# Optimization experiments

Measured on AMD Instinct MI355X. Metric: run time of the kernel, lower is better.

## Reference

```python
import jax, jax.numpy as jnp
import numpy as np

IMG = 2048
STRIDES = [8, 16, 32, 64, 128]
A = 9                       # num_cell_anchors
CLASS_NUM = 16              # num_classes - 1
TOPK = 1000                 # config.test_layer_topk
MAX_DELTA = float(np.log(1000.0 / 16.0))

_LEVEL_N = [(IMG // s) * (IMG // s) * A for s in STRIDES]


def setup_inputs() -> dict:
    key = jax.random.key(0)
    inp = {}
    for l, n in enumerate(_LEVEL_N):
        key, k1, k2, k3, k4 = jax.random.split(key, 5)
        cxcy = jax.random.uniform(k1, (n, 2), minval=0.0, maxval=float(IMG))
        wh = jax.random.uniform(k2, (n, 2), minval=8.0, maxval=128.0)
        inp[f"anchors{l}"] = jnp.concatenate([cxcy - 0.5 * wh, cxcy + 0.5 * wh], axis=1)
        # logits biased negative like a trained RetinaNet cls head (prior_prob init)
        inp[f"cls{l}"] = jax.random.normal(k3, (1, n, CLASS_NUM), dtype=jnp.float32) - 4.0
        inp[f"reg{l}"] = jax.random.normal(k4, (1, n, 8), dtype=jnp.float32) * 0.1
    return inp


def bbox_transform_inv(rois, deltas):
    # standard box decode (restore_bbox with unnormalize=False)
    w = rois[:, 2] - rois[:, 0]
    h = rois[:, 3] - rois[:, 1]
    cx = rois[:, 0] + 0.5 * w
    cy = rois[:, 1] + 0.5 * h
    pcx = cx + deltas[:, 0] * w
    pcy = cy + deltas[:, 1] * h
    pw = w * jnp.exp(jnp.minimum(deltas[:, 2], MAX_DELTA))
    ph = h * jnp.exp(jnp.minimum(deltas[:, 3], MAX_DELTA))
    return jnp.stack([pcx - 0.5 * pw, pcy - 0.5 * ph,
                      pcx + 0.5 * pw, pcy + 0.5 * ph], axis=1)


def _per_layer(anchors, pred_cls, pred_reg):
    a = anchors.reshape(-1, 4)
    c = pred_cls[0].reshape(-1, CLASS_NUM)
    r = pred_reg[0].reshape(-1, 8)[:, :4]
    if a.shape[0] > TOPK:
        ruler = jnp.max(c, axis=1)                  # max score over classes
        _, inds = jax.lax.top_k(ruler, TOPK)        # irregular topk + gather
        a = jnp.take(a, inds, axis=0)
        c = jnp.take(c, inds, axis=0)
        r = jnp.take(r, inds, axis=0)
    return a, jax.nn.sigmoid(c), r


def reference(anchors0, cls0, reg0, anchors1, cls1, reg1, anchors2, cls2, reg2,
              anchors3, cls3, reg3, anchors4, cls4, reg4):
    levels = [(anchors0, cls0, reg0), (anchors1, cls1, reg1),
              (anchors2, cls2, reg2), (anchors3, cls3, reg3),
              (anchors4, cls4, reg4)]
    kept = [_per_layer(a, c, r) for a, c, r in levels]
    keep_anchors = jnp.concatenate([k[0] for k in kept], axis=0)   # [K,4]
    keep_cls = jnp.concatenate([k[1] for k in kept], axis=0)       # [K,C]
    keep_reg = jnp.concatenate([k[2] for k in kept], axis=0)       # [K,4]
    K = keep_cls.shape[0]
    tag = jnp.tile(jnp.arange(CLASS_NUM, dtype=keep_cls.dtype) + 1.0, (K,)).reshape(-1, 1)
    pred_scores = keep_cls.reshape(-1, 1)                          # [K*C,1]
    pred_bbox = bbox_transform_inv(keep_anchors, keep_reg)         # [K,4]
    pred_bbox = jnp.tile(pred_bbox, (1, CLASS_NUM)).reshape(-1, 4) # [K*C,4]
    return jnp.concatenate([pred_bbox, pred_scores, tag], axis=1)  # [K*C,6]
```

## Files before the change

### kernel.cpp

```cpp
#include <hip/hip_runtime.h>
#include <math.h>

#define NLEV 5
#define TOPKK 1000
#define NCLS 16
#define NPART 16
#define PART_CAP 256
#define CAND_TOT 2048
#define NTOT 785664u
#define HISTSZ (NLEV * 256)

__device__ __forceinline__ int find_level(unsigned i, unsigned& loc) {
    if (i < 589824u) { loc = i;            return 0; }
    if (i < 737280u) { loc = i - 589824u;  return 1; }
    if (i < 774144u) { loc = i - 737280u;  return 2; }
    if (i < 783360u) { loc = i - 774144u;  return 3; }
    loc = i - 783360u; return 4;
}

struct Ptrs {
    const float* anc[NLEV];
    const float* cls[NLEV];
    const float* reg[NLEV];
};

__device__ __forceinline__ unsigned f2key(float f) {
    unsigned u = __float_as_uint(f);
    return (u & 0x80000000u) ? ~u : (u | 0x80000000u);
}

__device__ __forceinline__ float max4(float4 v) {
    return fmaxf(fmaxf(v.x, v.y), fmaxf(v.z, v.w));
}

__global__ void k_keys_hist(Ptrs p, unsigned* keys, unsigned* hist) {
    __shared__ unsigned lh[HISTSZ];
    for (int t = threadIdx.x; t < HISTSZ; t += blockDim.x) lh[t] = 0u;
    __syncthreads();
    unsigned i = blockIdx.x * blockDim.x + threadIdx.x;
    if (i < NTOT) {
        unsigned loc; int l = find_level(i, loc);
        const float4* c = (const float4*)(p.cls[l]) + (size_t)loc * 4;
        float4 a = c[0], b = c[1], d = c[2], e = c[3];
        float m = max4(a);
        m = fmaxf(m, max4(b));
        m = fmaxf(m, max4(d));
        m = fmaxf(m, max4(e));
        unsigned k = f2key(m);
        keys[i] = k;
        atomicAdd(&lh[l * 256 + (k >> 24)], 1u);
    }
    __syncthreads();
    unsigned part = blockIdx.x & (NPART - 1);
    for (int t = threadIdx.x; t < HISTSZ; t += blockDim.x)
        if (lh[t]) atomicAdd(&hist[part * HISTSZ + t], lh[t]);
}

__global__ void k_hist2(const unsigned* keys, const unsigned* prefix, unsigned* hist) {
    __shared__ unsigned lh[HISTSZ];
    __shared__ unsigned pf[NLEV];
    for (int t = threadIdx.x; t < HISTSZ; t += blockDim.x) lh[t] = 0u;
    if (threadIdx.x < NLEV) pf[threadIdx.x] = prefix[threadIdx.x];
    __syncthreads();
    unsigned i = blockIdx.x * blockDim.x + threadIdx.x;
    if (i < NTOT) {
        unsigned loc; int l = find_level(i, loc);
        unsigned k = keys[i];
        if ((k & 0xFF000000u) == pf[l])
            atomicAdd(&lh[l * 256 + ((k >> 16) & 0xFFu)], 1u);
    }
    __syncthreads();
    unsigned part = blockIdx.x & (NPART - 1);
    for (int t = threadIdx.x; t < HISTSZ; t += blockDim.x)
        if (lh[t]) atomicAdd(&hist[part * HISTSZ + t], lh[t]);
}

__global__ void k_select(unsigned* hist, unsigned* prefix, unsigned* remaining,
                         int shift, int first, unsigned* zbuf, unsigned zn) {
    __shared__ unsigned s[256];
    int l = blockIdx.x;
    int t = threadIdx.x, r = 255 - t;
    unsigned c = 0;
    #pragma unroll
    for (int pp = 0; pp < NPART; pp++) c += hist[pp * HISTSZ + l * 256 + t];
    s[r] = c;
    __syncthreads();
    for (int d = 1; d < 256; d <<= 1) {
        unsigned v = (r >= d) ? s[r - d] : 0u;
        __syncthreads();
        s[r] += v;
        __syncthreads();
    }
    unsigned incl = s[r], above = incl - c;
    unsigned rem = first ? (unsigned)TOPKK : remaining[l];
    unsigned pf = first ? 0u : prefix[l];
    if (above < rem && rem <= incl) {
        prefix[l] = pf | (((unsigned)t) << shift);
        remaining[l] = rem - above;
    }
    for (unsigned i = blockIdx.x * 256u + t; i < zn; i += NLEV * 256u)
        zbuf[i] = 0u;
}

__global__ void k_compact(const unsigned* keys, const unsigned* prefix,
                          unsigned* cnt, unsigned long long* cand) {
    unsigned i = blockIdx.x * blockDim.x + threadIdx.x;
    if (i >= NTOT) return;
    unsigned loc; int l = find_level(i, loc);
    unsigned k = keys[i];
    if (k >= prefix[l]) {
        unsigned part = blockIdx.x & (NPART - 1);
        unsigned slot = atomicAdd(&cnt[l * NPART + part], 1u);
        if (slot < PART_CAP)
            cand[((size_t)(l * NPART + part)) * PART_CAP + slot] =
                ((unsigned long long)k << 32) | (unsigned)(~loc);
    }
}

__global__ __launch_bounds__(256) void k_rank_emit(Ptrs p, const unsigned* cnt,
                                                   const unsigned long long* cand,
                                                   float* out) {
    const float MAXD = 4.135166556742356f;
    int l = blockIdx.x >> 3;
    unsigned sl = blockIdx.x & 7;
    int t = threadIdx.x;
    __shared__ unsigned long long lbuf[CAND_TOT];
    __shared__ unsigned aux[33];

    if (t < NPART) {
        unsigned cc = cnt[l * NPART + t];
        aux[t] = (cc > PART_CAP) ? PART_CAP : cc;
    }
    __syncthreads();
    if (t == 0) {
        unsigned o = 0;
        for (int pp = 0; pp < NPART; pp++) { aux[16 + pp] = o; o += aux[pp]; }
        aux[32] = (o > CAND_TOT) ? CAND_TOT : o;
    }
    __syncthreads();
    unsigned n = aux[32];
    for (int pp = 0; pp < NPART; pp++) {
        unsigned cc = aux[pp], o = aux[16 + pp];
        for (unsigned e = t; e < cc; e += 256) {
            unsigned dst = o + e;
            if (dst < CAND_TOT)
                lbuf[dst] = cand[((size_t)(l * NPART + pp)) * PART_CAP + e];
        }
    }
    __syncthreads();

    unsigned j = sl * 256u + t;
    if (j >= n) return;
    unsigned long long my = lbuf[j];
    unsigned rank = 0;
    #pragma unroll 8
    for (unsigned q = 0; q < n; q++) rank += (lbuf[q] > my) ? 1u : 0u;
    if (rank >= TOPKK) return;

    unsigned idx = ~((unsigned)(my & 0xFFFFFFFFull));
    float4 an = ((const float4*)p.anc[l])[idx];
    float4 dd = ((const float4*)p.reg[l])[(size_t)idx * 2];
    float w = an.z - an.x, h = an.w - an.y;
    float cx = an.x + 0.5f * w, cy = an.y + 0.5f * h;
    float pcx = cx + dd.x * w, pcy = cy + dd.y * h;
    float pw = w * expf(fminf(dd.z, MAXD));
    float ph = h * expf(fminf(dd.w, MAXD));
    float bx = pcx - 0.5f * pw, by = pcy - 0.5f * ph;
    float bz = pcx + 0.5f * pw, bw = pcy + 0.5f * ph;

    const float4* cp = (const float4*)(p.cls[l]) + (size_t)idx * 4;
    float sg[16];
    #pragma unroll
    for (int g = 0; g < 4; g++) {
        float4 v = cp[g];
        sg[4 * g + 0] = 1.0f / (1.0f + expf(-v.x));
        sg[4 * g + 1] = 1.0f / (1.0f + expf(-v.y));
        sg[4 * g + 2] = 1.0f / (1.0f + expf(-v.z));
        sg[4 * g + 3] = 1.0f / (1.0f + expf(-v.w));
    }
    float4* q = (float4*)(out + (size_t)(l * TOPKK + rank) * (NCLS * 6));
    #pragma unroll
    for (int g = 0; g < 8; g++) {
        float ta = (float)(2 * g + 1), tb = (float)(2 * g + 2);
        q[3 * g + 0] = make_float4(bx, by, bz, bw);
        q[3 * g + 1] = make_float4(sg[2 * g], ta, bx, by);
        q[3 * g + 2] = make_float4(bz, bw, sg[2 * g + 1], tb);
    }
}

extern "C" void kernel_launch(void* const* d_in, const int* in_sizes, int n_in,
                              void* d_out, int out_size, void* d_ws, size_t ws_size,
                              hipStream_t stream) {
    Ptrs p;
    for (int l = 0; l < NLEV; l++) {
        p.anc[l] = (const float*)d_in[3 * l + 0];
        p.cls[l] = (const float*)d_in[3 * l + 1];
        p.reg[l] = (const float*)d_in[3 * l + 2];
    }
    char* w = (char*)d_ws;
    unsigned* keys      = (unsigned*)w;
    unsigned* histA     = (unsigned*)(w + 3142656);
    unsigned* histB     = (unsigned*)(w + 3224576);
    unsigned long long* cand = (unsigned long long*)(w + 3306496);
    unsigned* prefix    = (unsigned*)(w + 3470336);
    unsigned* remaining = (unsigned*)(w + 3470368);
    unsigned* cnt       = (unsigned*)(w + 3470400);

    float* out = (float*)d_out;
    int nb = (NTOT + 255) / 256;

    (void)hipMemsetAsync(histA, 0, 81920, stream);
    k_keys_hist<<<nb, 256, 0, stream>>>(p, keys, histA);
    k_select<<<NLEV, 256, 0, stream>>>(histA, prefix, remaining, 24, 1,
                                       histB, HISTSZ * NPART);
    k_hist2<<<nb, 256, 0, stream>>>(keys, prefix, histB);
    k_select<<<NLEV, 256, 0, stream>>>(histB, prefix, remaining, 16, 0,
                                       cnt, NLEV * NPART);
    k_compact<<<nb, 256, 0, stream>>>(keys, prefix, cnt, cand);
    k_rank_emit<<<NLEV * 8, 256, 0, stream>>>(p, cnt, cand, out);
}
```

Baseline: 195.9 us.

## Fold radix-select scans into histogram and compaction kernels, dropping two select launches

Removes the two small single-wave k_select launches. Each block of the hist2 and compact kernels now redundantly recomputes the per-level prefix scan from the global histograms. One memset clears histA, histB and the counters together. Because every level size is a multiple of 256, each block belongs to exactly one level, so the local histogram shrinks to 256 bins and the bounds checks go away. The cost is that every one of about three thousand blocks reads 16x256 histogram entries and runs a 256-wide scan, twice in compact.

```diff
diff --git a/kernel.cpp b/kernel.cpp
--- a/kernel.cpp
+++ b/kernel.cpp
@@ -33,56 +33,13 @@
     return fmaxf(fmaxf(v.x, v.y), fmaxf(v.z, v.w));
 }
 
-__global__ void k_keys_hist(Ptrs p, unsigned* keys, unsigned* hist) {
-    __shared__ unsigned lh[HISTSZ];
-    for (int t = threadIdx.x; t < HISTSZ; t += blockDim.x) lh[t] = 0u;
-    __syncthreads();
-    unsigned i = blockIdx.x * blockDim.x + threadIdx.x;
-    if (i < NTOT) {
-        unsigned loc; int l = find_level(i, loc);
-        const float4* c = (const float4*)(p.cls[l]) + (size_t)loc * 4;
-        float4 a = c[0], b = c[1], d = c[2], e = c[3];
-        float m = max4(a);
-        m = fmaxf(m, max4(b));
-        m = fmaxf(m, max4(d));
-        m = fmaxf(m, max4(e));
-        unsigned k = f2key(m);
-        keys[i] = k;
-        atomicAdd(&lh[l * 256 + (k >> 24)], 1u);
-    }
-    __syncthreads();
-    unsigned part = blockIdx.x & (NPART - 1);
-    for (int t = threadIdx.x; t < HISTSZ; t += blockDim.x)
-        if (lh[t]) atomicAdd(&hist[part * HISTSZ + t], lh[t]);
-}
-
-__global__ void k_hist2(const unsigned* keys, const unsigned* prefix, unsigned* hist) {
-    __shared__ unsigned lh[HISTSZ];
-    __shared__ unsigned pf[NLEV];
-    for (int t = threadIdx.x; t < HISTSZ; t += blockDim.x) lh[t] = 0u;
-    if (threadIdx.x < NLEV) pf[threadIdx.x] = prefix[threadIdx.x];
-    __syncthreads();
-    unsigned i = blockIdx.x * blockDim.x + threadIdx.x;
-    if (i < NTOT) {
-        unsigned loc; int l = find_level(i, loc);
-        unsigned k = keys[i];
-        if ((k & 0xFF000000u) == pf[l])
-            atomicAdd(&lh[l * 256 + ((k >> 16) & 0xFFu)], 1u);
-    }
-    __syncthreads();
-    unsigned part = blockIdx.x & (NPART - 1);
-    for (int t = threadIdx.x; t < HISTSZ; t += blockDim.x)
-        if (lh[t]) atomicAdd(&hist[part * HISTSZ + t], lh[t]);
-}
-
-__global__ void k_select(unsigned* hist, unsigned* prefix, unsigned* remaining,
-                         int shift, int first, unsigned* zbuf, unsigned zn) {
-    __shared__ unsigned s[256];
-    int l = blockIdx.x;
+__device__ void level_select(const unsigned* histbase, int l, int shift,
+                             unsigned rem_in, unsigned pf_acc,
+                             unsigned* s, unsigned* aux) {
     int t = threadIdx.x, r = 255 - t;
     unsigned c = 0;
     #pragma unroll
-    for (int pp = 0; pp < NPART; pp++) c += hist[pp * HISTSZ + l * 256 + t];
+    for (int pp = 0; pp < NPART; pp++) c += histbase[pp * HISTSZ + l * 256 + t];
     s[r] = c;
     __syncthreads();
     for (int d = 1; d < 256; d <<= 1) {
@@ -92,23 +49,73 @@
         __syncthreads();
     }
     unsigned incl = s[r], above = incl - c;
-    unsigned rem = first ? (unsigned)TOPKK : remaining[l];
-    unsigned pf = first ? 0u : prefix[l];
-    if (above < rem && rem <= incl) {
-        prefix[l] = pf | (((unsigned)t) << shift);
-        remaining[l] = rem - above;
-    }
-    for (unsigned i = blockIdx.x * 256u + t; i < zn; i += NLEV * 256u)
-        zbuf[i] = 0u;
-}
-
-__global__ void k_compact(const unsigned* keys, const unsigned* prefix,
-                          unsigned* cnt, unsigned long long* cand) {
-    unsigned i = blockIdx.x * blockDim.x + threadIdx.x;
-    if (i >= NTOT) return;
+    if (above < rem_in && rem_in <= incl) {
+        aux[0] = pf_acc | (((unsigned)t) << shift);
+        aux[1] = rem_in - above;
+    }
+    __syncthreads();
+}
+
+__global__ __launch_bounds__(256) void k_keys_hist(Ptrs p, unsigned* keys,
+                                                   unsigned* hist) {
+    __shared__ unsigned lh[256];
+    lh[threadIdx.x] = 0u;
+    __syncthreads();
+    unsigned i = blockIdx.x * 256u + threadIdx.x;
     unsigned loc; int l = find_level(i, loc);
-    unsigned k = keys[i];
-    if (k >= prefix[l]) {
+    const float4* c = (const float4*)(p.cls[l]) + (size_t)loc * 4;
+    float4 a = c[0], b = c[1], d = c[2], e = c[3];
+    float m = max4(a);
+    m = fmaxf(m, max4(b));
+    m = fmaxf(m, max4(d));
+    m = fmaxf(m, max4(e));
+    unsigned k = f2key(m);
+    keys[i] = k;
+    atomicAdd(&lh[k >> 24], 1u);
+    __syncthreads();
+    unsigned part = blockIdx.x & (NPART - 1);
+    if (lh[threadIdx.x])
+        atomicAdd(&hist[part * HISTSZ + l * 256 + threadIdx.x], lh[threadIdx.x]);
+}
+
+__global__ __launch_bounds__(256) void k_hist2(const unsigned* keys,
+                                               const unsigned* histA,
+                                               unsigned* histB) {
+    __shared__ unsigned s[256];
+    __shared__ unsigned lh[256];
+    __shared__ unsigned aux[2];
+    unsigned i0 = blockIdx.x * 256u;
+    unsigned loc0; int l = find_level(i0, loc0);
+    level_select(histA, l, 24, TOPKK, 0u, s, aux);
+    unsigned pf = aux[0];
+    lh[threadIdx.x] = 0u;
+    __syncthreads();
+    unsigned k = keys[i0 + threadIdx.x];
+    if ((k & 0xFF000000u) == pf)
+        atomicAdd(&lh[(k >> 16) & 0xFFu], 1u);
+    __syncthreads();
+    unsigned part = blockIdx.x & (NPART - 1);
+    if (lh[threadIdx.x])
+        atomicAdd(&histB[part * HISTSZ + l * 256 + threadIdx.x], lh[threadIdx.x]);
+}
+
+__global__ __launch_bounds__(256) void k_compact(const unsigned* keys,
+                                                 const unsigned* histA,
+                                                 const unsigned* histB,
+                                                 unsigned* cnt,
+                                                 unsigned long long* cand) {
+    __shared__ unsigned s[256];
+    __shared__ unsigned aux[2];
+    unsigned i0 = blockIdx.x * 256u;
+    unsigned loc0; int l = find_level(i0, loc0);
+    level_select(histA, l, 24, TOPKK, 0u, s, aux);
+    unsigned pf1 = aux[0], rem1 = aux[1];
+    __syncthreads();
+    level_select(histB, l, 16, rem1, pf1, s, aux);
+    unsigned thresh = aux[0];
+    unsigned k = keys[i0 + threadIdx.x];
+    if (k >= thresh) {
+        unsigned loc = loc0 + threadIdx.x;
         unsigned part = blockIdx.x & (NPART - 1);
         unsigned slot = atomicAdd(&cnt[l * NPART + part], 1u);
         if (slot < PART_CAP)
@@ -198,24 +205,18 @@
         p.reg[l] = (const float*)d_in[3 * l + 2];
     }
     char* w = (char*)d_ws;
-    unsigned* keys      = (unsigned*)w;
-    unsigned* histA     = (unsigned*)(w + 3142656);
-    unsigned* histB     = (unsigned*)(w + 3224576);
-    unsigned long long* cand = (unsigned long long*)(w + 3306496);
-    unsigned* prefix    = (unsigned*)(w + 3470336);
-    unsigned* remaining = (unsigned*)(w + 3470368);
-    unsigned* cnt       = (unsigned*)(w + 3470400);
+    unsigned* keys  = (unsigned*)w;
+    unsigned* histA = (unsigned*)(w + 3142656);
+    unsigned* histB = (unsigned*)(w + 3224576);
+    unsigned* cnt   = (unsigned*)(w + 3306496);
+    unsigned long long* cand = (unsigned long long*)(w + 3306816);
 
     float* out = (float*)d_out;
-    int nb = (NTOT + 255) / 256;
-
-    (void)hipMemsetAsync(histA, 0, 81920, stream);
+    int nb = NTOT / 256;
+
+    (void)hipMemsetAsync(histA, 0, 164160, stream);
     k_keys_hist<<<nb, 256, 0, stream>>>(p, keys, histA);
-    k_select<<<NLEV, 256, 0, stream>>>(histA, prefix, remaining, 24, 1,
-                                       histB, HISTSZ * NPART);
-    k_hist2<<<nb, 256, 0, stream>>>(keys, prefix, histB);
-    k_select<<<NLEV, 256, 0, stream>>>(histB, prefix, remaining, 16, 0,
-                                       cnt, NLEV * NPART);
-    k_compact<<<nb, 256, 0, stream>>>(keys, prefix, cnt, cand);
+    k_hist2<<<nb, 256, 0, stream>>>(keys, histA, histB);
+    k_compact<<<nb, 256, 0, stream>>>(keys, histA, histB, cnt, cand);
     k_rank_emit<<<NLEV * 8, 256, 0, stream>>>(p, cnt, cand, out);
 }
```

Result: faster. 187.5 us (-4.3%).
